# Optimization experiments

Measured on AMD Instinct MI355X. Metric: run time of the kernel, lower is better.

Reference implementation:

```python
import jax, jax.numpy as jnp
import numpy as np

N = 100000   # nodes
E = 1200000  # edges
IN = 11      # input node feature dim (Linear(11, dim_h))
DIM = 64     # dim_h
G = 1000     # graphs in batch
BN_EPS = 1e-5


def setup_inputs() -> dict:
    key = jax.random.key(0)
    ks = jax.random.split(key, 40)
    rn = lambda k, s: jax.random.normal(k, s, dtype=jnp.float32) * 0.05
    inp = {}
    inp['x'] = jax.random.normal(ks[0], (N, IN), dtype=jnp.float32)
    inp['edge_index'] = jax.random.randint(ks[1], (2, E), 0, N)
    inp['batch'] = jnp.sort(jax.random.randint(ks[2], (N,), 0, G))
    i = 3
    for l, din in zip((1, 2, 3), (IN, DIM, DIM)):
        inp[f'w{l}a'] = rn(ks[i], (din, DIM)); i += 1
        inp[f'b{l}a'] = rn(ks[i], (DIM,)); i += 1
        inp[f'g{l}'] = 1.0 + rn(ks[i], (DIM,)); i += 1   # BN gamma
        inp[f'be{l}'] = rn(ks[i], (DIM,)); i += 1          # BN beta
        inp[f'm{l}'] = rn(ks[i], (DIM,)); i += 1           # BN running mean
        inp[f'v{l}'] = jax.random.uniform(ks[i], (DIM,), dtype=jnp.float32, minval=0.5, maxval=1.5); i += 1  # BN running var
        inp[f'w{l}b'] = rn(ks[i], (DIM, DIM)); i += 1
        inp[f'b{l}b'] = rn(ks[i], (DIM,)); i += 1
    inp['lw1'] = rn(ks[i], (DIM, DIM)); i += 1
    inp['lb1'] = rn(ks[i], (DIM,)); i += 1
    inp['lw2'] = rn(ks[i], (DIM, 1)); i += 1
    inp['lb2'] = rn(ks[i], (1,))
    return inp


def _bn(x, g, b, m, v):
    # BatchNorm1d in eval mode: running stats
    return (x - m) * jax.lax.rsqrt(v + BN_EPS) * g + b


def _gin_conv(h, src, dst, wa, ba, g, be, m, v, wb, bb):
    # GINConv eps=0: (1+eps)*x_i + sum_{j->i} x_j, then MLP
    agg = h + jax.ops.segment_sum(h[src], dst, num_segments=N)
    h1 = jax.nn.relu(_bn(agg @ wa + ba, g, be, m, v))
    return jax.nn.relu(h1 @ wb + bb)


def reference(x, edge_index, batch,
              w1a, b1a, g1, be1, m1, v1, w1b, b1b,
              w2a, b2a, g2, be2, m2, v2, w2b, b2b,
              w3a, b3a, g3, be3, m3, v3, w3b, b3b,
              lw1, lb1, lw2, lb2):
    src, dst = edge_index[0], edge_index[1]
    h = _gin_conv(x, src, dst, w1a, b1a, g1, be1, m1, v1, w1b, b1b)
    h = jax.nn.relu(h)  # matches h.relu() in forward (idempotent after MLP ReLU)
    h = _gin_conv(h, src, dst, w2a, b2a, g2, be2, m2, v2, w2b, b2b)
    h = jax.nn.relu(h)
    h = _gin_conv(h, src, dst, w3a, b3a, g3, be3, m3, v3, w3b, b3b)
    hg = jax.ops.segment_sum(h, batch, num_segments=G)  # global_add_pool -> [G, DIM]
    hg = jax.nn.relu(hg @ lw1 + lb1)
    # dropout p=0.1 is identity in eval mode
    return hg @ lw2 + lb2  # [G, 1]
```

## Files before the change

kernel.cpp:

```cpp
#include <hip/hip_runtime.h>


#define BN_EPS 1e-5f
#define NBUCK 512
#define NBLK  256

typedef __attribute__((ext_vector_type(8))) _Float16 half8v;
typedef __attribute__((ext_vector_type(4))) _Float16 half4v;
typedef __attribute__((ext_vector_type(4))) float float4v;

__global__ __launch_bounds__(256)
void setup_kernel(const int* __restrict__ dst, int* __restrict__ ghist,
                  int E, int chunk, _Float16* __restrict__ yrow,
                  const int* __restrict__ batch, int* __restrict__ gptr,
                  int N, int G,
                  const float* __restrict__ w0, const float* __restrict__ w1,
                  const float* __restrict__ w2, const float* __restrict__ w3,
                  const float* __restrict__ w4, _Float16* __restrict__ fwout) {
    __shared__ int h[NBUCK];
    const int blk = blockIdx.x, tid = threadIdx.x;

    if (blk < NBLK) {
        if (blk == 0 && tid < 64) yrow[tid] = (_Float16)0.f;
        for (int u = tid; u < NBUCK; u += 256) h[u] = 0;
        __syncthreads();
        const int e0 = blk * chunk, e1 = min(E, e0 + chunk);
        for (int e = e0 + tid; e < e1; e += 256)
            atomicAdd(&h[dst[e] >> 8], 1);
        __syncthreads();
        for (int u = tid; u < NBUCK; u += 256)
            ghist[u * NBLK + blk] = h[u];
    } else if (blk < NBLK + 5) {
        const int m = blk - NBLK;
        const float* w = (m == 0) ? w0 : (m == 1) ? w1 : (m == 2) ? w2 :
                         (m == 3) ? w3 : w4;
        _Float16* o = fwout + (size_t)m * 4096;
        const int lane = tid & 63;
        const int cb   = tid >> 6;
        const int half = lane >> 4, sub = lane & 15;
        #pragma unroll
        for (int it = 0; it < 2; ++it) {
            int c = cb + 4 * it;
            int kk = c >> 2, nt = c & 3;
            _Float16 f[8];
            #pragma unroll
            for (int j = 0; j < 8; ++j)
                f[j] = (_Float16)w[(kk * 32 + half * 8 + j) * 64 + nt * 16 + sub];
            *(half8v*)&o[((size_t)c * 64 + lane) * 8] = *(half8v*)f;
        }
    } else {
        int i = (blk - NBLK - 5) * 256 + tid;
        if (i < N) {
            int b = batch[i];
            int bprev = (i == 0) ? -1 : batch[i - 1];
            for (int g = bprev + 1; g <= b; ++g) gptr[g] = i;
            if (i == N - 1)
                for (int g = b + 1; g <= G; ++g) gptr[g] = N;
        }
    }
}

__global__ __launch_bounds__(256)
void scan_block_g(int* __restrict__ a, int* __restrict__ bsum, int n) {
    __shared__ int s[256];
    int i = blockIdx.x * 256 + threadIdx.x;
    int v = (i < n) ? a[i] : 0;
    s[threadIdx.x] = v;
    __syncthreads();
    for (int off = 1; off < 256; off <<= 1) {
        int t = (threadIdx.x >= off) ? s[threadIdx.x - off] : 0;
        __syncthreads();
        s[threadIdx.x] += t;
        __syncthreads();
    }
    if (i < n) a[i] = s[threadIdx.x] - v;
    if (threadIdx.x == 255) bsum[blockIdx.x] = s[255];
}

__global__ __launch_bounds__(512)
void scan_top_kernel(int* bsum, int nb) {
    __shared__ int s[512];
    int v = (threadIdx.x < nb) ? bsum[threadIdx.x] : 0;
    s[threadIdx.x] = v;
    __syncthreads();
    for (int off = 1; off < 512; off <<= 1) {
        int t = (threadIdx.x >= off) ? s[threadIdx.x - off] : 0;
        __syncthreads();
        s[threadIdx.x] += t;
        __syncthreads();
    }
    if (threadIdx.x < nb) bsum[threadIdx.x] = s[threadIdx.x] - v;
}

__global__ __launch_bounds__(256)
void bin_fill_kernel(const int* __restrict__ src, const int* __restrict__ dst,
                     const int* __restrict__ ghist, const int* __restrict__ bsum,
                     unsigned* __restrict__ pairs, int E, int chunk) {
    __shared__ int cur[NBUCK];
    const int tid = threadIdx.x, blk = blockIdx.x;
    for (int u = tid; u < NBUCK; u += 256)
        cur[u] = ghist[u * NBLK + blk] + bsum[u];
    __syncthreads();
    const int e0 = blk * chunk, e1 = min(E, e0 + chunk);
    for (int e = e0 + tid; e < e1; e += 256) {
        int d = dst[e];
        int pos = atomicAdd(&cur[d >> 8], 1);
        pairs[pos] = ((unsigned)(d & 255) << 24) | (unsigned)src[e];
    }
}

__global__ __launch_bounds__(256)
void csr_sort_kernel(const unsigned* __restrict__ pairs, const int* __restrict__ bsum,
                     int* __restrict__ col, int* __restrict__ rp,
                     int N, int E, int nbuckUsed) {
    __shared__ int cnt[256];
    __shared__ int cur[256];
    const int u = blockIdx.x, tid = threadIdx.x;
    const int base = bsum[u];
    const int end  = (u == NBUCK - 1) ? E : bsum[u + 1];
    const int node0 = u << 8;
    const int rows = min(256, N - node0);

    cnt[tid] = 0;
    __syncthreads();
    for (int e = base + tid; e < end; e += 256)
        atomicAdd(&cnt[pairs[e] >> 24], 1);
    __syncthreads();
    int own = cnt[tid];
    __syncthreads();
    cnt[tid] = own;
    __syncthreads();
    for (int off = 1; off < 256; off <<= 1) {
        int t = (tid >= off) ? cnt[tid - off] : 0;
        __syncthreads();
        cnt[tid] += t;
        __syncthreads();
    }
    const int excl = cnt[tid] - own;
    if (tid < rows) rp[node0 + tid] = base + excl;
    if (tid == 0 && u == nbuckUsed - 1) rp[N] = E;
    cur[tid] = base + excl;
    __syncthreads();
    for (int e = base + tid; e < end; e += 256) {
        unsigned p = pairs[e];
        int pos = atomicAdd(&cur[p >> 24], 1);
        col[pos] = (int)(p & 0xFFFFFF);
    }
}

__global__ __launch_bounds__(256)
void pre_kernel(const float* __restrict__ x, const float* __restrict__ wa,
                _Float16* __restrict__ yh, int n) {
    __shared__ float s_wa[11 * 64];
    __shared__ float s_row[4][11];
    const int tid = threadIdx.x;
    const int lane = tid & 63;
    const int local = tid >> 6;
    for (int i = tid; i < 11 * 64; i += 256) s_wa[i] = wa[i];
    __syncthreads();
    const int groups = (n + 3) >> 2;
    for (int grp = blockIdx.x; grp < groups; grp += gridDim.x) {
        const int node = grp * 4 + local;
        if (node >= n) continue;
        if (lane < 11) s_row[local][lane] = x[(size_t)node * 11 + lane];
        float acc = 0.f;
        #pragma unroll
        for (int k = 0; k < 11; ++k)
            acc = fmaf(s_row[local][k], s_wa[k * 64 + lane], acc);
        yh[((size_t)node << 6) + lane] = (_Float16)acc;
    }
}

__global__ __launch_bounds__(256, 8)
void agg_kernel(const _Float16* __restrict__ yh, const int* __restrict__ rp,
                const int* __restrict__ col,
                const float* __restrict__ ba,
                const float* __restrict__ gam, const float* __restrict__ bet,
                const float* __restrict__ rm, const float* __restrict__ rv,
                _Float16* __restrict__ th, int n) {
    const int wv   = (blockIdx.x << 2) | (threadIdx.x >> 6);
    const int lane = threadIdx.x & 63;
    const int grp  = lane >> 4;
    const int gl   = lane & 15;
    const int node = (wv << 2) | grp;
    if (node >= n) return;
    const int fo = gl << 2;

    const int beg = rp[node], end = rp[node + 1];

    half4v selfv = *(const half4v*)&yh[((size_t)node << 6) + fo];
    float a0 = (float)selfv[0], a1 = (float)selfv[1];
    float a2 = (float)selfv[2], a3 = (float)selfv[3];

    for (int i = beg; i < end; i += 16) {
        int c[16];
        half4v v[16];
        #pragma unroll
        for (int j = 0; j < 16; ++j) c[j] = (i + j < end) ? col[i + j] : n;
        #pragma unroll
        for (int j = 0; j < 16; ++j)
            v[j] = *(const half4v*)&yh[((size_t)c[j] << 6) + fo];
        #pragma unroll
        for (int j = 0; j < 16; ++j) {
            a0 += (float)v[j][0];
            a1 += (float)v[j][1];
            a2 += (float)v[j][2];
            a3 += (float)v[j][3];
        }
    }

    const float4 g4 = *(const float4*)&gam[fo];
    const float4 v4 = *(const float4*)&rv[fo];
    const float4 b4 = *(const float4*)&bet[fo];
    const float4 m4 = *(const float4*)&rm[fo];
    const float4 ba4 = *(const float4*)&ba[fo];
    const float s0 = g4.x * rsqrtf(v4.x + BN_EPS);
    const float s1 = g4.y * rsqrtf(v4.y + BN_EPS);
    const float s2 = g4.z * rsqrtf(v4.z + BN_EPS);
    const float s3 = g4.w * rsqrtf(v4.w + BN_EPS);
    half4v o;
    o[0] = (_Float16)fmaxf(fmaf(a0, s0, b4.x - m4.x * s0 + ba4.x * s0), 0.f);
    o[1] = (_Float16)fmaxf(fmaf(a1, s1, b4.y - m4.y * s1 + ba4.y * s1), 0.f);
    o[2] = (_Float16)fmaxf(fmaf(a2, s2, b4.z - m4.z * s2 + ba4.z * s2), 0.f);
    o[3] = (_Float16)fmaxf(fmaf(a3, s3, b4.w - m4.w * s3 + ba4.w * s3), 0.f);
    *(half4v*)&th[((size_t)node << 6) + fo] = o;
}

template<bool LAST>
__global__ __launch_bounds__(256, 2)
void mlp_mfma_kernel(const _Float16* __restrict__ th,
                     const _Float16* __restrict__ fwb,
                     const float* __restrict__ bb,
                     const _Float16* __restrict__ fwn,
                     _Float16* __restrict__ outh, int n) {
    __shared__ _Float16 zt[4][16][72];

    const int tid  = threadIdx.x;
    const int lane = tid & 63;
    const int w    = tid >> 6;
    const int half = lane >> 4;
    const int sub  = lane & 15;

    half8v wbf[2][4];
    #pragma unroll
    for (int kk = 0; kk < 2; ++kk)
        #pragma unroll
        for (int nt = 0; nt < 4; ++nt)
            wbf[kk][nt] = *(const half8v*)&fwb[(((size_t)(kk * 4 + nt)) * 64 + lane) * 8];
    half8v wnf[LAST ? 1 : 2][4];
    if (!LAST) {
        #pragma unroll
        for (int kk = 0; kk < 2; ++kk)
            #pragma unroll
            for (int nt = 0; nt < 4; ++nt)
                wnf[kk][nt] = *(const half8v*)&fwn[(((size_t)(kk * 4 + nt)) * 64 + lane) * 8];
    }
    float bbr[4];
    #pragma unroll
    for (int nt = 0; nt < 4; ++nt) bbr[nt] = bb[nt * 16 + sub];

    const int ngroups = (n + 15) >> 4;
    const int stride = gridDim.x * 4;
    for (int group = blockIdx.x * 4 + w; group < ngroups; group += stride) {
        const int node0 = group << 4;
        int mrow = node0 + sub;
        if (mrow >= n) mrow = n - 1;

        half8v at[2];
        #pragma unroll
        for (int kk = 0; kk < 2; ++kk)
            at[kk] = *(const half8v*)&th[((size_t)mrow << 6) + kk * 32 + half * 8];

        float4v accz[4];
        #pragma unroll
        for (int nt = 0; nt < 4; ++nt) {
            float4v c = {0.f, 0.f, 0.f, 0.f};
            c = __builtin_amdgcn_mfma_f32_16x16x32_f16(at[0], wbf[0][nt], c, 0, 0, 0);
            c = __builtin_amdgcn_mfma_f32_16x16x32_f16(at[1], wbf[1][nt], c, 0, 0, 0);
            accz[nt] = c;
        }

        if (LAST) {
            #pragma unroll
            for (int nt = 0; nt < 4; ++nt)
                #pragma unroll
                for (int r = 0; r < 4; ++r) {
                    int m = node0 + half * 4 + r;
                    if (m < n)
                        outh[((size_t)m << 6) + nt * 16 + sub] =
                            (_Float16)fmaxf(accz[nt][r] + bbr[nt], 0.f);
                }
        } else {
            #pragma unroll
            for (int nt = 0; nt < 4; ++nt)
                #pragma unroll
                for (int r = 0; r < 4; ++r)
                    zt[w][half * 4 + r][nt * 16 + sub] =
                        (_Float16)fmaxf(accz[nt][r] + bbr[nt], 0.f);
            asm volatile("s_waitcnt lgkmcnt(0)" ::: "memory");
            __builtin_amdgcn_sched_barrier(0);
            half8v az[2];
            #pragma unroll
            for (int kk = 0; kk < 2; ++kk)
                az[kk] = *(const half8v*)&zt[w][sub][kk * 32 + half * 8];

            #pragma unroll
            for (int nt = 0; nt < 4; ++nt) {
                float4v c = {0.f, 0.f, 0.f, 0.f};
                c = __builtin_amdgcn_mfma_f32_16x16x32_f16(az[0], wnf[0][nt], c, 0, 0, 0);
                c = __builtin_amdgcn_mfma_f32_16x16x32_f16(az[1], wnf[1][nt], c, 0, 0, 0);
                #pragma unroll
                for (int r = 0; r < 4; ++r) {
                    int m = node0 + half * 4 + r;
                    if (m < n)
                        outh[((size_t)m << 6) + nt * 16 + sub] = (_Float16)c[r];
                }
            }
        }
    }
}

__global__ __launch_bounds__(64)
void pool_head_kernel(const _Float16* __restrict__ h, const int* __restrict__ gptr,
                      const float* __restrict__ lw1, const float* __restrict__ lb1,
                      const float* __restrict__ lw2, const float* __restrict__ lb2,
                      float* __restrict__ out, int G) {
    __shared__ float s_row[64];
    const int g = blockIdx.x;
    if (g >= G) return;
    const int d = threadIdx.x;
    const int beg = gptr[g], end = gptr[g + 1];

    float acc = 0.f;
    int i = beg;
    const int end8 = beg + ((end - beg) & ~7);
    for (; i < end8; i += 8) {
        float v[8];
        #pragma unroll
        for (int j = 0; j < 8; ++j)
            v[j] = (float)h[((size_t)(i + j) << 6) + d];
        #pragma unroll
        for (int j = 0; j < 8; ++j) acc += v[j];
    }
    for (; i < end; ++i) acc += (float)h[((size_t)i << 6) + d];

    s_row[d] = acc;
    __syncthreads();

    float z = lb1[d];
    #pragma unroll 8
    for (int k = 0; k < 64; ++k)
        z = fmaf(s_row[k], lw1[k * 64 + d], z);
    z = fmaxf(z, 0.f);
    float r = z * lw2[d];
    #pragma unroll
    for (int off = 32; off > 0; off >>= 1)
        r += __shfl_down(r, off, 64);
    if (d == 0) out[g] = r + lb2[0];
}

extern "C" void kernel_launch(void* const* d_in, const int* in_sizes, int n_in,
                              void* d_out, int out_size, void* d_ws, size_t ws_size,
                              hipStream_t stream) {
    const float* x    = (const float*)d_in[0];
    const int* ei     = (const int*)d_in[1];
    const int* batch  = (const int*)d_in[2];
    const int N = in_sizes[0] / 11;
    const int E = in_sizes[1] / 2;
    const int G = out_size;
    const int* src = ei;
    const int* dst = ei + E;

    const float* p[28];
    for (int i = 0; i < 28; ++i) p[i] = (const float*)d_in[3 + i];

    _Float16* yh  = (_Float16*)d_ws;
    _Float16* th  = yh + ((size_t)N + 1) * 64;
    _Float16* h3h = th + (size_t)N * 64;
    _Float16* fw  = h3h + (size_t)N * 64;
    int*   ghist  = (int*)(fw + 5 * 4096);
    int*   bsum   = ghist + NBUCK * NBLK;
    int*   rp     = bsum + 512;
    int*   gptr   = rp + N + 1;
    int*   col    = gptr + G + 1;
    unsigned* pairs = (unsigned*)(col + E);

    const int chunk     = (E + NBLK - 1) / NBLK;
    const int nscan     = NBUCK * NBLK;
    const int nbScanB   = nscan / 256;
    const int nbuckUsed = (N + 255) >> 8;
    const int nWaves    = (N + 3) / 4;
    const int nbAgg     = (nWaves + 3) / 4;
    const int nGptrBlocks = (N + 255) / 256;

    _Float16* fwb1 = fw;
    _Float16* fwn1 = fw + 4096;
    _Float16* fwb2 = fw + 2 * 4096;
    _Float16* fwn2 = fw + 3 * 4096;
    _Float16* fwb3 = fw + 4 * 4096;

    setup_kernel<<<NBLK + 5 + nGptrBlocks, 256, 0, stream>>>(
        dst, ghist, E, chunk, yh + (size_t)N * 64,
        batch, gptr, N, G,
        p[6], p[8], p[14], p[16], p[22], fw);

    scan_block_g<<<nbScanB, 256, 0, stream>>>(ghist, bsum, nscan);
    scan_top_kernel<<<1, 512, 0, stream>>>(bsum, nbScanB);
    bin_fill_kernel<<<NBLK, 256, 0, stream>>>(src, dst, ghist, bsum, pairs, E, chunk);
    csr_sort_kernel<<<nbuckUsed, 256, 0, stream>>>(pairs, bsum, col, rp, N, E, nbuckUsed);

    pre_kernel<<<2048, 256, 0, stream>>>(x, p[0], yh, N);

    agg_kernel<<<nbAgg, 256, 0, stream>>>(yh, rp, col, p[1], p[2], p[3], p[4], p[5], th, N);
    mlp_mfma_kernel<false><<<1024, 256, 0, stream>>>(th, fwb1, p[7], fwn1, yh, N);
    agg_kernel<<<nbAgg, 256, 0, stream>>>(yh, rp, col, p[9], p[10], p[11], p[12], p[13], th, N);
    mlp_mfma_kernel<false><<<1024, 256, 0, stream>>>(th, fwb2, p[15], fwn2, yh, N);
    agg_kernel<<<nbAgg, 256, 0, stream>>>(yh, rp, col, p[17], p[18], p[19], p[20], p[21], th, N);
    mlp_mfma_kernel<true><<<1024, 256, 0, stream>>>(th, fwb3, p[23], nullptr, h3h, N);

    pool_head_kernel<<<G, 64, 0, stream>>>(h3h, gptr,
        p[24], p[25], p[26], p[27], (float*)d_out, G);
}
```

Measured before the change: 184.5 us.

## Fuse neighbor aggregation with MFMA MLP into a per-layer kernel via LDS staging

Merges the gather/BN/ReLU aggregation kernel and the MFMA MLP kernel into one layer_kernel. Each wave aggregates a 16-node tile into shared memory and feeds it straight to the MFMA stage, so the intermediate th buffer is no longer written to and read back from global memory and three launches are saved. Buffers now ping-pong between yA and yB, each with a zero pad row. The cost is lower occupancy (launch bounds 3 vs 8 for aggregation), a fixed 1024-block grid, a gather unroll cut from 16 to 8, and aggregation latency that each wave must now hide alongside matrix work.

```diff
diff --git a/kernel.cpp b/kernel.cpp
--- a/kernel.cpp
+++ b/kernel.cpp
@@ -11,7 +11,8 @@
 
 __global__ __launch_bounds__(256)
 void setup_kernel(const int* __restrict__ dst, int* __restrict__ ghist,
-                  int E, int chunk, _Float16* __restrict__ yrow,
+                  int E, int chunk,
+                  _Float16* __restrict__ padA, _Float16* __restrict__ padB,
                   const int* __restrict__ batch, int* __restrict__ gptr,
                   int N, int G,
                   const float* __restrict__ w0, const float* __restrict__ w1,
@@ -21,7 +22,10 @@
     const int blk = blockIdx.x, tid = threadIdx.x;
 
     if (blk < NBLK) {
-        if (blk == 0 && tid < 64) yrow[tid] = (_Float16)0.f;
+        if (blk == 0 && tid < 64) {
+            padA[tid] = (_Float16)0.f;
+            padB[tid] = (_Float16)0.f;
+        }
         for (int u = tid; u < NBUCK; u += 256) h[u] = 0;
         __syncthreads();
         const int e0 = blk * chunk, e1 = min(E, e0 + chunk);
@@ -171,43 +175,45 @@
     }
 }
 
-__global__ __launch_bounds__(256, 8)
-void agg_kernel(const _Float16* __restrict__ yh, const int* __restrict__ rp,
-                const int* __restrict__ col,
-                const float* __restrict__ ba,
-                const float* __restrict__ gam, const float* __restrict__ bet,
-                const float* __restrict__ rm, const float* __restrict__ rv,
-                _Float16* __restrict__ th, int n) {
-    const int wv   = (blockIdx.x << 2) | (threadIdx.x >> 6);
-    const int lane = threadIdx.x & 63;
-    const int grp  = lane >> 4;
-    const int gl   = lane & 15;
-    const int node = (wv << 2) | grp;
-    if (node >= n) return;
-    const int fo = gl << 2;
-
-    const int beg = rp[node], end = rp[node + 1];
-
-    half4v selfv = *(const half4v*)&yh[((size_t)node << 6) + fo];
-    float a0 = (float)selfv[0], a1 = (float)selfv[1];
-    float a2 = (float)selfv[2], a3 = (float)selfv[3];
-
-    for (int i = beg; i < end; i += 16) {
-        int c[16];
-        half4v v[16];
-        #pragma unroll
-        for (int j = 0; j < 16; ++j) c[j] = (i + j < end) ? col[i + j] : n;
-        #pragma unroll
-        for (int j = 0; j < 16; ++j)
-            v[j] = *(const half4v*)&yh[((size_t)c[j] << 6) + fo];
-        #pragma unroll
-        for (int j = 0; j < 16; ++j) {
-            a0 += (float)v[j][0];
-            a1 += (float)v[j][1];
-            a2 += (float)v[j][2];
-            a3 += (float)v[j][3];
-        }
-    }
+template<bool LAST>
+__global__ __launch_bounds__(256, 3)
+void layer_kernel(const _Float16* __restrict__ yh,
+                  const int* __restrict__ rp, const int* __restrict__ col,
+                  const float* __restrict__ ba,
+                  const float* __restrict__ gam, const float* __restrict__ bet,
+                  const float* __restrict__ rm, const float* __restrict__ rv,
+                  const _Float16* __restrict__ fwb,
+                  const float* __restrict__ bb,
+                  const _Float16* __restrict__ fwn,
+                  _Float16* __restrict__ outh,
+                  int n) {
+    __shared__ _Float16 tt[4][16][72];
+    __shared__ _Float16 zt[4][16][72];
+
+    const int tid  = threadIdx.x;
+    const int lane = tid & 63;
+    const int w    = tid >> 6;
+    const int half = lane >> 4;
+    const int sub  = lane & 15;
+    const int fo   = sub << 2;
+
+    half8v wbf[2][4];
+    #pragma unroll
+    for (int kk = 0; kk < 2; ++kk)
+        #pragma unroll
+        for (int nt = 0; nt < 4; ++nt)
+            wbf[kk][nt] = *(const half8v*)&fwb[(((size_t)(kk * 4 + nt)) * 64 + lane) * 8];
+    half8v wnf[LAST ? 1 : 2][4];
+    if (!LAST) {
+        #pragma unroll
+        for (int kk = 0; kk < 2; ++kk)
+            #pragma unroll
+            for (int nt = 0; nt < 4; ++nt)
+                wnf[kk][nt] = *(const half8v*)&fwn[(((size_t)(kk * 4 + nt)) * 64 + lane) * 8];
+    }
+    float bbr[4];
+    #pragma unroll
+    for (int nt = 0; nt < 4; ++nt) bbr[nt] = bb[nt * 16 + sub];
 
     const float4 g4 = *(const float4*)&gam[fo];
     const float4 v4 = *(const float4*)&rv[fo];
@@ -218,58 +224,58 @@
     const float s1 = g4.y * rsqrtf(v4.y + BN_EPS);
     const float s2 = g4.z * rsqrtf(v4.z + BN_EPS);
     const float s3 = g4.w * rsqrtf(v4.w + BN_EPS);
-    half4v o;
-    o[0] = (_Float16)fmaxf(fmaf(a0, s0, b4.x - m4.x * s0 + ba4.x * s0), 0.f);
-    o[1] = (_Float16)fmaxf(fmaf(a1, s1, b4.y - m4.y * s1 + ba4.y * s1), 0.f);
-    o[2] = (_Float16)fmaxf(fmaf(a2, s2, b4.z - m4.z * s2 + ba4.z * s2), 0.f);
-    o[3] = (_Float16)fmaxf(fmaf(a3, s3, b4.w - m4.w * s3 + ba4.w * s3), 0.f);
-    *(half4v*)&th[((size_t)node << 6) + fo] = o;
-}
-
-template<bool LAST>
-__global__ __launch_bounds__(256, 2)
-void mlp_mfma_kernel(const _Float16* __restrict__ th,
-                     const _Float16* __restrict__ fwb,
-                     const float* __restrict__ bb,
-                     const _Float16* __restrict__ fwn,
-                     _Float16* __restrict__ outh, int n) {
-    __shared__ _Float16 zt[4][16][72];
-
-    const int tid  = threadIdx.x;
-    const int lane = tid & 63;
-    const int w    = tid >> 6;
-    const int half = lane >> 4;
-    const int sub  = lane & 15;
-
-    half8v wbf[2][4];
-    #pragma unroll
-    for (int kk = 0; kk < 2; ++kk)
-        #pragma unroll
-        for (int nt = 0; nt < 4; ++nt)
-            wbf[kk][nt] = *(const half8v*)&fwb[(((size_t)(kk * 4 + nt)) * 64 + lane) * 8];
-    half8v wnf[LAST ? 1 : 2][4];
-    if (!LAST) {
+    const float h0 = b4.x - m4.x * s0 + ba4.x * s0;
+    const float h1 = b4.y - m4.y * s1 + ba4.y * s1;
+    const float h2 = b4.z - m4.z * s2 + ba4.z * s2;
+    const float h3 = b4.w - m4.w * s3 + ba4.w * s3;
+
+    const int ntiles = (n + 15) >> 4;
+    const int stride = gridDim.x * 4;
+    for (int tile = blockIdx.x * 4 + w; tile < ntiles; tile += stride) {
+        const int node0 = tile << 4;
+
+        for (int p = 0; p < 4; ++p) {
+            const int r = p * 4 + half;
+            const int node = node0 + r;
+            const bool ok = (node < n);
+            const int nodeg = ok ? node : n;
+            const int beg = ok ? rp[node] : 0;
+            const int end = ok ? rp[node + 1] : 0;
+
+            half4v selfv = *(const half4v*)&yh[((size_t)nodeg << 6) + fo];
+            float a0 = (float)selfv[0], a1 = (float)selfv[1];
+            float a2 = (float)selfv[2], a3 = (float)selfv[3];
+
+            for (int i = beg; i < end; i += 8) {
+                int c[8];
+                half4v v[8];
+                #pragma unroll
+                for (int j = 0; j < 8; ++j) c[j] = (i + j < end) ? col[i + j] : n;
+                #pragma unroll
+                for (int j = 0; j < 8; ++j)
+                    v[j] = *(const half4v*)&yh[((size_t)c[j] << 6) + fo];
+                #pragma unroll
+                for (int j = 0; j < 8; ++j) {
+                    a0 += (float)v[j][0];
+                    a1 += (float)v[j][1];
+                    a2 += (float)v[j][2];
+                    a3 += (float)v[j][3];
+                }
+            }
+            half4v o;
+            o[0] = (_Float16)fmaxf(fmaf(a0, s0, h0), 0.f);
+            o[1] = (_Float16)fmaxf(fmaf(a1, s1, h1), 0.f);
+            o[2] = (_Float16)fmaxf(fmaf(a2, s2, h2), 0.f);
+            o[3] = (_Float16)fmaxf(fmaf(a3, s3, h3), 0.f);
+            *(half4v*)&tt[w][r][fo] = o;
+        }
+        asm volatile("s_waitcnt lgkmcnt(0)" ::: "memory");
+        __builtin_amdgcn_sched_barrier(0);
+
+        half8v at[2];
         #pragma unroll
         for (int kk = 0; kk < 2; ++kk)
-            #pragma unroll
-            for (int nt = 0; nt < 4; ++nt)
-                wnf[kk][nt] = *(const half8v*)&fwn[(((size_t)(kk * 4 + nt)) * 64 + lane) * 8];
-    }
-    float bbr[4];
-    #pragma unroll
-    for (int nt = 0; nt < 4; ++nt) bbr[nt] = bb[nt * 16 + sub];
-
-    const int ngroups = (n + 15) >> 4;
-    const int stride = gridDim.x * 4;
-    for (int group = blockIdx.x * 4 + w; group < ngroups; group += stride) {
-        const int node0 = group << 4;
-        int mrow = node0 + sub;
-        if (mrow >= n) mrow = n - 1;
-
-        half8v at[2];
-        #pragma unroll
-        for (int kk = 0; kk < 2; ++kk)
-            at[kk] = *(const half8v*)&th[((size_t)mrow << 6) + kk * 32 + half * 8];
+            at[kk] = *(const half8v*)&tt[w][sub][kk * 32 + half * 8];
 
         float4v accz[4];
         #pragma unroll
@@ -374,10 +380,9 @@
     const float* p[28];
     for (int i = 0; i < 28; ++i) p[i] = (const float*)d_in[3 + i];
 
-    _Float16* yh  = (_Float16*)d_ws;
-    _Float16* th  = yh + ((size_t)N + 1) * 64;
-    _Float16* h3h = th + (size_t)N * 64;
-    _Float16* fw  = h3h + (size_t)N * 64;
+    _Float16* yA  = (_Float16*)d_ws;
+    _Float16* yB  = yA + ((size_t)N + 1) * 64;
+    _Float16* fw  = yB + ((size_t)N + 1) * 64;
     int*   ghist  = (int*)(fw + 5 * 4096);
     int*   bsum   = ghist + NBUCK * NBLK;
     int*   rp     = bsum + 512;
@@ -389,8 +394,6 @@
     const int nscan     = NBUCK * NBLK;
     const int nbScanB   = nscan / 256;
     const int nbuckUsed = (N + 255) >> 8;
-    const int nWaves    = (N + 3) / 4;
-    const int nbAgg     = (nWaves + 3) / 4;
     const int nGptrBlocks = (N + 255) / 256;
 
     _Float16* fwb1 = fw;
@@ -400,7 +403,8 @@
     _Float16* fwb3 = fw + 4 * 4096;
 
     setup_kernel<<<NBLK + 5 + nGptrBlocks, 256, 0, stream>>>(
-        dst, ghist, E, chunk, yh + (size_t)N * 64,
+        dst, ghist, E, chunk,
+        yA + (size_t)N * 64, yB + (size_t)N * 64,
         batch, gptr, N, G,
         p[6], p[8], p[14], p[16], p[22], fw);
 
@@ -409,15 +413,15 @@
     bin_fill_kernel<<<NBLK, 256, 0, stream>>>(src, dst, ghist, bsum, pairs, E, chunk);
     csr_sort_kernel<<<nbuckUsed, 256, 0, stream>>>(pairs, bsum, col, rp, N, E, nbuckUsed);
 
-    pre_kernel<<<2048, 256, 0, stream>>>(x, p[0], yh, N);
-
-    agg_kernel<<<nbAgg, 256, 0, stream>>>(yh, rp, col, p[1], p[2], p[3], p[4], p[5], th, N);
-    mlp_mfma_kernel<false><<<1024, 256, 0, stream>>>(th, fwb1, p[7], fwn1, yh, N);
-    agg_kernel<<<nbAgg, 256, 0, stream>>>(yh, rp, col, p[9], p[10], p[11], p[12], p[13], th, N);
-    mlp_mfma_kernel<false><<<1024, 256, 0, stream>>>(th, fwb2, p[15], fwn2, yh, N);
-    agg_kernel<<<nbAgg, 256, 0, stream>>>(yh, rp, col, p[17], p[18], p[19], p[20], p[21], th, N);
-    mlp_mfma_kernel<true><<<1024, 256, 0, stream>>>(th, fwb3, p[23], nullptr, h3h, N);
-
-    pool_head_kernel<<<G, 64, 0, stream>>>(h3h, gptr,
+    pre_kernel<<<2048, 256, 0, stream>>>(x, p[0], yA, N);
+
+    layer_kernel<false><<<1024, 256, 0, stream>>>(yA, rp, col,
+        p[1], p[2], p[3], p[4], p[5], fwb1, p[7], fwn1, yB, N);
+    layer_kernel<false><<<1024, 256, 0, stream>>>(yB, rp, col,
+        p[9], p[10], p[11], p[12], p[13], fwb2, p[15], fwn2, yA, N);
+    layer_kernel<true><<<1024, 256, 0, stream>>>(yA, rp, col,
+        p[17], p[18], p[19], p[20], p[21], fwb3, p[23], nullptr, yB, N);
+
+    pool_head_kernel<<<G, 64, 0, stream>>>(yB, gptr,
         p[24], p[25], p[26], p[27], (float*)d_out, G);
 }
```

New measurement: 166.6 us. -9.7%, faster.
